# Kernel tuning notes

Measured on AMD Instinct MI355X. Metric: run time of the kernel, lower is better.

Reference implementation:

```python
import jax, jax.numpy as jnp
import numpy as np

# Module hyperparameters (from init_kwargs)
IOU_T = 0.5
PROB_T = 0.75
COV = 10.0
TOPK = 500       # self.topk
PRE_K = 2048     # fixed-shape cap on post-threshold candidates entering NMS
B, C, H, W = 4, 4, 160, 160


def setup_inputs() -> dict:
    key = jax.random.key(0)
    k1, k2 = jax.random.split(key)
    mask = jax.random.normal(k1, (B, C, H, W), dtype=jnp.float32)
    # scale bias so boxes have ~10px extent (realistic detections)
    bias = jax.random.normal(k2, (B, 4, H, W), dtype=jnp.float32) * 8.0
    return {"mask": mask, "bias": bias}


def _pos_grid(h, w):
    # equivalent of np.dstack(np.mgrid[0:h, 0:w]) -> [h, w, 2] with (y, x)
    yy, xx = jnp.meshgrid(jnp.arange(h), jnp.arange(w), indexing="ij")
    return jnp.stack([yy, xx], axis=-1).astype(jnp.float32)


def _pairwise_iou(b):
    # b: [K, 4] as (y1, x1, y2, x2); torchvision-style IoU (areas unclamped, inter clamped)
    area = (b[:, 2] - b[:, 0]) * (b[:, 3] - b[:, 1])
    lt = jnp.maximum(b[:, None, :2], b[None, :, :2])
    rb = jnp.minimum(b[:, None, 2:], b[None, :, 2:])
    wh = jnp.clip(rb - lt, 0.0)
    inter = wh[..., 0] * wh[..., 1]
    return inter / (area[:, None] + area[None, :] - inter)


def _nms_keep(iou, valid, thresh):
    # boxes are pre-sorted by descending score; greedy suppression
    K = iou.shape[0]
    idx = jnp.arange(K)
    def body(i, keep):
        sup = (iou[i] > thresh) & (idx > i) & keep[i]
        return keep & ~sup
    return jax.lax.fori_loop(0, K, body, valid)


def _per_image(mask_i, bias_i, pos):
    # mask_i: [C, h, w], bias_i: [4, h, w], pos: [h, w, 2]
    p = jax.nn.softmax(mask_i, axis=0)
    prob = jax.lax.stop_gradient(p.max(axis=0))          # prob.detach()
    cls = p.argmax(axis=0)
    frontal = (cls != 0) & (prob > PROB_T)               # [h, w]
    # boxes = pos tiled to (y,x,y,x) + bias.permute(0,2,3,1)
    boxes = jnp.concatenate([pos, pos], axis=-1) + jnp.transpose(bias_i, (1, 2, 0))
    boxes = boxes.reshape(-1, 4)                          # [h*w, 4]
    score = jnp.where(frontal.reshape(-1), prob.reshape(-1), -1.0)
    # fixed-size candidate set, sorted by descending score (invalid -> -1)
    top_s, idx = jax.lax.top_k(score, PRE_K)
    cand = boxes[idx]
    valid = top_s > 0.0                                   # valid scores > PROB_T > 0
    keep = _nms_keep(_pairwise_iou(cand), valid, IOU_T)
    kept_s = jnp.where(keep, top_s, -1.0)
    fin_s, fi = jax.lax.top_k(kept_s, TOPK)               # min(topk, n) via padding
    fboxes = cand[fi]                                     # [TOPK, 4]
    fvalid = fin_s > 0.0
    fprob = jnp.where(fvalid, fin_s, 0.0)
    mu = (fboxes[:, :2] + fboxes[:, 2:]) * 0.5            # [TOPK, 2]
    sigma = fboxes[:, 2:] - fboxes[:, :2]
    sigma = jnp.where(fvalid[:, None], sigma, 1.0)        # safe divisor for padding
    # gaussian2d: z = (pos - mu) / (sigma / cov); heat = max_n exp(-|z|^2/2) * prob
    z = (pos[None] - mu[:, None, None, :]) / (sigma[:, None, None, :] / COV)  # [TOPK,h,w,2]
    g = jnp.exp(-0.5 * (z ** 2).sum(axis=-1)) * fprob[:, None, None]
    heat = g.max(axis=0)                                  # [h, w]; all-padded -> 0, matches n==0 case
    return heat, fboxes, fvalid


def reference(mask, bias):
    pos = _pos_grid(mask.shape[2], mask.shape[3])
    heat, fboxes, fvalid = jax.vmap(lambda m, b: _per_image(m, b, pos))(mask, bias)
    # original returns (heatmaps, mask, boxes); boxes padded to [B, TOPK, 4] with validity mask
    return heat, mask, fboxes, fvalid
```

## Files before the change

### kernel.cpp

```cpp
#include <hip/hip_runtime.h>
#include <math.h>

#define BATCH 4
#define NCH 4
#define H 160
#define W 160
#define NPIX (H * W)
#define PRE_K 2048
#define TOPK 500
#define PROB_T 0.75f
#define IOU_T 0.5f
#define COV 10.0f

#define SCORE_OFF 0u
#define FS_OFF    409600u
#define FIDX_OFF  819200u
#define F_OFF     1228800u
#define CIDX_OFF  1228864u
#define CSC_OFF   1261632u
#define CBOX_OFF  1294400u
#define SUP_OFF   1425472u
#define KEEP_OFF  3522624u
#define NV_OFF    3523648u
#define PAR_OFF   3523712u
#define FLAG_OFF  3563712u

#define OUT_HEAT_OFF 0
#define OUT_MASK_OFF 102400
#define OUT_BOX_OFF  512000
#define OUT_VAL_OFF  520000

typedef unsigned long long u64;
typedef unsigned int u32;

__device__ __forceinline__ int block_scan_excl(int v, int tid, int* tmp, int* total) {
    tmp[tid] = v;
    __syncthreads();
    for (int off = 1; off < 256; off <<= 1) {
        int y = (tid >= off) ? tmp[tid - off] : 0;
        __syncthreads();
        tmp[tid] += y;
        __syncthreads();
    }
    int incl = tmp[tid];
    *total = tmp[255];
    __syncthreads();
    return incl - v;
}

__global__ void k_score(const float* __restrict__ mask, float* __restrict__ score) {
    int b = blockIdx.y;
    int pix = blockIdx.x * 256 + threadIdx.x;
    const float* mp = mask + (size_t)b * NCH * NPIX + pix;
    float x0 = mp[0], x1 = mp[NPIX], x2 = mp[2 * NPIX], x3 = mp[3 * NPIX];
    float m = x0; int c = 0;
    if (x1 > m) { m = x1; c = 1; }
    if (x2 > m) { m = x2; c = 2; }
    if (x3 > m) { m = x3; c = 3; }
    float sum = ((expf(x0 - m) + expf(x1 - m)) + expf(x2 - m)) + expf(x3 - m);
    float prob = 1.0f / sum;
    bool frontal = (c != 0) && (prob > PROB_T);
    score[(size_t)b * NPIX + pix] = frontal ? prob : -1.0f;
}

#define PPT (NPIX / 1024)
__global__ void __launch_bounds__(1024)
k_compact(const float* __restrict__ score, float* __restrict__ fs,
          int* __restrict__ fidx, int* __restrict__ Fout,
          int* __restrict__ cand_idx, float* __restrict__ cand_score) {
    int b = blockIdx.x;
    int tid = threadIdx.x;
    const float* sc = score + (size_t)b * NPIX;
    int p0 = tid * PPT;
    float v[PPT];
    int cnt = 0;
    #pragma unroll
    for (int j = 0; j < PPT; ++j) {
        v[j] = sc[p0 + j];
        cnt += (v[j] > 0.0f) ? 1 : 0;
    }
    int lane = tid & 63, wv = tid >> 6;
    int incl = cnt;
    for (int off = 1; off < 64; off <<= 1) {
        int y = __shfl_up(incl, off);
        if (lane >= off) incl += y;
    }
    __shared__ int wtot[16];
    __shared__ int wpre[17];
    if (lane == 63) wtot[wv] = incl;
    __syncthreads();
    if (tid == 0) {
        int acc = 0;
        for (int k = 0; k < 16; ++k) { wpre[k] = acc; acc += wtot[k]; }
        wpre[16] = acc;
    }
    __syncthreads();
    int f_excl = wpre[wv] + (incl - cnt);
    int F = wpre[16];
    if (tid == 0) Fout[b] = F;
    int w = f_excl;
    #pragma unroll
    for (int j = 0; j < PPT; ++j) {
        if (v[j] > 0.0f) {
            fs[(size_t)b * NPIX + w] = v[j];
            fidx[(size_t)b * NPIX + w] = p0 + j;
            ++w;
        }
    }
    if (F < PRE_K) {
        int slot = F + (p0 - f_excl);
        if (slot < PRE_K) {
            #pragma unroll
            for (int j = 0; j < PPT; ++j) {
                if (!(v[j] > 0.0f)) {
                    if (slot < PRE_K) {
                        cand_idx[(size_t)b * PRE_K + slot] = p0 + j;
                        cand_score[(size_t)b * PRE_K + slot] = -1.0f;
                    }
                    ++slot;
                }
            }
        }
    }
}

__global__ void k_rank(const float* __restrict__ fs, const int* __restrict__ fidx,
                       const int* __restrict__ Fout, int* __restrict__ cand_idx,
                       float* __restrict__ cand_score) {
    int b = blockIdx.y;
    int F = Fout[b];
    if (blockIdx.x * 256 >= F) return;
    int i = blockIdx.x * 256 + threadIdx.x;
    bool act = i < F;
    float si = 0.0f; int xi = 0;
    if (act) { si = fs[(size_t)b * NPIX + i]; xi = fidx[(size_t)b * NPIX + i]; }
    int rank = 0;
    __shared__ float ls[256];
    __shared__ int li[256];
    for (int base = 0; base < F; base += 256) {
        int j = base + threadIdx.x;
        if (j < F) { ls[threadIdx.x] = fs[(size_t)b * NPIX + j]; li[threadIdx.x] = fidx[(size_t)b * NPIX + j]; }
        __syncthreads();
        int lim = min(256, F - base);
        if (act) {
            for (int k = 0; k < lim; ++k) {
                float sj = ls[k]; int xj = li[k];
                rank += (sj > si || (sj == si && xj < xi)) ? 1 : 0;
            }
        }
        __syncthreads();
    }
    if (act && rank < PRE_K) {
        cand_idx[(size_t)b * PRE_K + rank] = xi;
        cand_score[(size_t)b * PRE_K + rank] = si;
    }
}

__global__ void k_boxes(const float* __restrict__ bias, const int* __restrict__ cand_idx,
                        float* __restrict__ cand_box) {
    int t = blockIdx.x * 256 + threadIdx.x;
    int b = t >> 11;
    int s = t & (PRE_K - 1);
    int pix = cand_idx[(size_t)b * PRE_K + s];
    float y = (float)(pix / W), x = (float)(pix % W);
    const float* bb = bias + (size_t)b * 4 * NPIX;
    float4 box;
    box.x = y + bb[0 * NPIX + pix];
    box.y = x + bb[1 * NPIX + pix];
    box.z = y + bb[2 * NPIX + pix];
    box.w = x + bb[3 * NPIX + pix];
    ((float4*)cand_box)[(size_t)b * PRE_K + s] = box;
}

__global__ void __launch_bounds__(512)
k_iou(const float* __restrict__ cand_box, u32* __restrict__ sup,
      unsigned char* __restrict__ flag) {
    int b = blockIdx.y;
    int r0 = blockIdx.x * 8;
    __shared__ float ly1[PRE_K], lx1[PRE_K], ly2[PRE_K], lx2[PRE_K], lar[PRE_K];
    for (int k = threadIdx.x; k < PRE_K; k += 512) {
        float4 v = ((const float4*)cand_box)[(size_t)b * PRE_K + k];
        ly1[k] = v.x; lx1[k] = v.y; ly2[k] = v.z; lx2[k] = v.w;
        lar[k] = (v.z - v.x) * (v.w - v.y);
    }
    __syncthreads();
    int lr = threadIdx.x >> 6;
    int w = threadIdx.x & 63;
    int i = r0 + lr;
    float ay1 = ly1[i], ax1 = lx1[i], ay2 = ly2[i], ax2 = lx2[i], aa = lar[i];
    u32 bits = 0;
    int jbase = w * 32;
    #pragma unroll 4
    for (int jj = 0; jj < 32; ++jj) {
        int jo = (jj + w) & 31;
        int j = jbase + jo;
        if (j > i) {
            float lty = fmaxf(ay1, ly1[j]);
            float ltx = fmaxf(ax1, lx1[j]);
            float rby = fminf(ay2, ly2[j]);
            float rbx = fminf(ax2, lx2[j]);
            float wy = fmaxf(rby - lty, 0.0f);
            float wx = fmaxf(rbx - ltx, 0.0f);
            float inter = wy * wx;
            float iou = inter / ((aa + lar[j]) - inter);
            if (iou > IOU_T) bits |= (1u << jo);
        }
    }
    sup[((size_t)b * PRE_K + i) * 64 + w] = bits;
    bool any = __any(bits != 0u);
    if (w == 0) flag[(size_t)b * PRE_K + i] = any ? 1 : 0;
}

__global__ void __launch_bounds__(64)
k_nms(const u32* __restrict__ sup, const unsigned char* __restrict__ flag,
      const int* __restrict__ Fout, u32* __restrict__ keep) {
    int b = blockIdx.x;
    int lane = threadIdx.x;
    int F = Fout[b];
    int V = F < PRE_K ? F : PRE_K;
    __shared__ int rid_s[PRE_K];

    const u32* f32 = (const u32*)(flag + (size_t)b * PRE_K);
    u32 fw[8];
    #pragma unroll
    for (int k = 0; k < 8; ++k) fw[k] = f32[lane * 8 + k];
    int r0 = lane * 32;
    int cnt = 0;
    #pragma unroll
    for (int k = 0; k < 8; ++k) {
        #pragma unroll
        for (int j = 0; j < 4; ++j) {
            int r = r0 + k * 4 + j;
            if (((fw[k] >> (8 * j)) & 0xFFu) != 0u && r < V) ++cnt;
        }
    }
    int incl = cnt;
    for (int off = 1; off < 64; off <<= 1) {
        int y = __shfl_up(incl, off);
        if (lane >= off) incl += y;
    }
    int M = __shfl(incl, 63);
    int pos = incl - cnt;
    #pragma unroll
    for (int k = 0; k < 8; ++k) {
        #pragma unroll
        for (int j = 0; j < 4; ++j) {
            int r = r0 + k * 4 + j;
            if (((fw[k] >> (8 * j)) & 0xFFu) != 0u && r < V) rid_s[pos++] = r;
        }
    }
    __syncthreads();

    int rem = V - lane * 32;
    u32 kw = (rem >= 32) ? 0xFFFFFFFFu : (rem <= 0 ? 0u : ((1u << rem) - 1u));

    const u32* supb = sup + (size_t)b * PRE_K * 64 + lane;
    int C = (M + 7) >> 3;
    int C4 = (C + 3) & ~3;
    int l7 = lane & 7;

    u32 rbuf[4][8];
    int ridv[4];

    #define LOAD_RID(slot, c) ridv[slot] = rid_s[min((c) * 8 + l7, PRE_K - 1)]
    #define ISSUE(slot) do { \
        _Pragma("unroll") \
        for (int k_ = 0; k_ < 8; ++k_) { \
            int i_ = __builtin_amdgcn_readlane(ridv[slot], k_) & (PRE_K - 1); \
            rbuf[slot][k_] = supb[(size_t)i_ * 64]; \
        } \
    } while (0)
    #define PROC(slot, c) do { \
        _Pragma("unroll") \
        for (int k_ = 0; k_ < 8; ++k_) { \
            int m_ = (c) * 8 + k_; \
            if (m_ < M) { \
                int i_ = __builtin_amdgcn_readlane(ridv[slot], k_) & (PRE_K - 1); \
                u32 kb_ = (u32)__builtin_amdgcn_readlane((int)kw, i_ >> 5); \
                if ((kb_ >> (i_ & 31)) & 1u) kw &= ~rbuf[slot][k_]; \
            } \
        } \
    } while (0)

    LOAD_RID(0, 0); LOAD_RID(1, 1); LOAD_RID(2, 2); LOAD_RID(3, 3);
    ISSUE(0); ISSUE(1); ISSUE(2);

    for (int c = 0; c < C4; c += 4) {
        PROC(0, c);     ISSUE(3);            LOAD_RID(0, c + 4);
        PROC(1, c + 1); ISSUE(0);            LOAD_RID(1, c + 5);
        PROC(2, c + 2); ISSUE(1);            LOAD_RID(2, c + 6);
        PROC(3, c + 3); ISSUE(2);            LOAD_RID(3, c + 7);
    }
    #undef LOAD_RID
    #undef ISSUE
    #undef PROC

    keep[(size_t)b * 64 + lane] = kw;
}

__global__ void k_finalize(const u32* __restrict__ keep, const float* __restrict__ cand_score,
                           const float* __restrict__ cand_box, float* __restrict__ out_boxes,
                           float* __restrict__ out_valid, float* __restrict__ params,
                           int* __restrict__ NV) {
    int b = blockIdx.x;
    int tid = threadIdx.x;
    __shared__ u32 kws[64];
    __shared__ int tmp[256];
    if (tid < 64) kws[tid] = keep[(size_t)b * 64 + tid];
    __syncthreads();
    int s0 = tid * 8;
    int bits8 = (int)((kws[s0 >> 5] >> (s0 & 31)) & 0xFFu);
    int cnt = __popc(bits8);
    int tot;
    int kpre = block_scan_excl(cnt, tid, tmp, &tot);
    int NK = tot;
    for (int k = 0; k < 8; ++k) {
        int s = s0 + k;
        int kept = (bits8 >> k) & 1;
        int pos = kept ? kpre : (NK + s - kpre);
        if (pos < TOPK) {
            float4 bx = ((const float4*)cand_box)[(size_t)b * PRE_K + s];
            ((float4*)out_boxes)[(size_t)b * TOPK + pos] = bx;
            out_valid[(size_t)b * TOPK + pos] = kept ? 1.0f : 0.0f;
            if (kept) {
                float scv = cand_score[(size_t)b * PRE_K + s];
                float* pp = params + ((size_t)b * TOPK + pos) * 5;
                pp[0] = (bx.x + bx.z) * 0.5f;
                pp[1] = (bx.y + bx.w) * 0.5f;
                pp[2] = (bx.z - bx.x) / COV;
                pp[3] = (bx.w - bx.y) / COV;
                pp[4] = scv;
            }
        }
        kpre += kept;
    }
    if (tid == 0) NV[b] = NK < TOPK ? NK : TOPK;
}

#define TILE 16
#define TPL (W / TILE)
__global__ void k_heat(const float* __restrict__ params, const int* __restrict__ NV,
                       float* __restrict__ heat) {
    int b = blockIdx.y;
    int ty0 = (blockIdx.x / TPL) * TILE;
    int tx0 = (blockIdx.x % TPL) * TILE;
    int tid = threadIdx.x;
    int nv = NV[b];
    __shared__ float lp[TOPK * 5];
    __shared__ int cntS;
    if (tid == 0) cntS = 0;
    __syncthreads();
    for (int t = tid; t < nv; t += 256) {
        const float* pp = params + ((size_t)b * TOPK + t) * 5;
        float muy = pp[0], mux = pp[1], dy = pp[2], dx = pp[3], p = pp[4];
        float cy = fmaxf(fmaxf((float)ty0 - muy, muy - (float)(ty0 + TILE - 1)), 0.0f);
        float cx = fmaxf(fmaxf((float)tx0 - mux, mux - (float)(tx0 + TILE - 1)), 0.0f);
        float zy = cy / fabsf(dy);
        float zx = cx / fabsf(dx);
        float z2 = zy * zy + zx * zx;
        if (!(z2 > 40.0f)) {
            int idx = atomicAdd(&cntS, 1);
            float* q = lp + idx * 5;
            q[0] = muy; q[1] = mux; q[2] = dy; q[3] = dx; q[4] = p;
        }
    }
    __syncthreads();
    int n = cntS;
    float py = (float)(ty0 + (tid >> 4));
    float px = (float)(tx0 + (tid & 15));
    float m = 0.0f;
    for (int t = 0; t < n; ++t) {
        float muy = lp[t * 5 + 0], mux = lp[t * 5 + 1];
        float dy = lp[t * 5 + 2], dx = lp[t * 5 + 3], p = lp[t * 5 + 4];
        float zy = (py - muy) / dy;
        float zx = (px - mux) / dx;
        float g = expf(-0.5f * (zy * zy + zx * zx)) * p;
        m = fmaxf(m, g);
    }
    heat[(size_t)b * NPIX + (ty0 + (tid >> 4)) * W + tx0 + (tid & 15)] = m;
}

extern "C" void kernel_launch(void* const* d_in, const int* in_sizes, int n_in,
                              void* d_out, int out_size, void* d_ws, size_t ws_size,
                              hipStream_t stream) {
    const float* mask = (const float*)d_in[0];
    const float* bias = (const float*)d_in[1];
    float* out = (float*)d_out;
    char* ws = (char*)d_ws;

    float* score      = (float*)(ws + SCORE_OFF);
    float* fs         = (float*)(ws + FS_OFF);
    int*   fidx       = (int*)(ws + FIDX_OFF);
    int*   Fout       = (int*)(ws + F_OFF);
    int*   cand_idx   = (int*)(ws + CIDX_OFF);
    float* cand_score = (float*)(ws + CSC_OFF);
    float* cand_box   = (float*)(ws + CBOX_OFF);
    u32*   sup        = (u32*)(ws + SUP_OFF);
    u32*   keep       = (u32*)(ws + KEEP_OFF);
    int*   NV         = (int*)(ws + NV_OFF);
    float* params     = (float*)(ws + PAR_OFF);
    unsigned char* flag = (unsigned char*)(ws + FLAG_OFF);

    hipMemcpyAsync(out + OUT_MASK_OFF, mask, (size_t)BATCH * NCH * NPIX * sizeof(float),
                   hipMemcpyDeviceToDevice, stream);

    dim3 g100(NPIX / 256, BATCH);
    k_score<<<g100, 256, 0, stream>>>(mask, score);
    k_compact<<<BATCH, 1024, 0, stream>>>(score, fs, fidx, Fout, cand_idx, cand_score);
    k_rank<<<g100, 256, 0, stream>>>(fs, fidx, Fout, cand_idx, cand_score);
    k_boxes<<<dim3(BATCH * PRE_K / 256), 256, 0, stream>>>(bias, cand_idx, cand_box);
    k_iou<<<dim3(PRE_K / 8, BATCH), 512, 0, stream>>>(cand_box, sup, flag);
    k_nms<<<BATCH, 64, 0, stream>>>(sup, flag, Fout, keep);
    k_finalize<<<BATCH, 256, 0, stream>>>(keep, cand_score, cand_box,
                                          out + OUT_BOX_OFF, out + OUT_VAL_OFF, params, NV);
    k_heat<<<dim3(TPL * (H / TILE), BATCH), 256, 0, stream>>>(params, NV, out + OUT_HEAT_OFF);
}
```

Baseline: 137.7 us.

## Fuse pipeline stages and drop memcpy, skip IoU rows beyond valid count

Folds the mask copy into the score kernel, merges compaction, ranking and box gathering into one per-image kernel that ranks candidates from LDS, and merges NMS with finalize. IoU blocks whose rows all fall past the valid candidate count now exit early. This cuts launches, intermediate global traffic and wasted IoU work. The cost is that ranking now runs in only one 1024-thread block per image, which serialises O(F^2) comparisons when there are many candidates.

```diff
diff --git a/kernel.cpp b/kernel.cpp
--- a/kernel.cpp
+++ b/kernel.cpp
@@ -11,6 +11,7 @@
 #define PROB_T 0.75f
 #define IOU_T 0.5f
 #define COV 10.0f
+#define CAP 4096
 
 #define SCORE_OFF 0u
 #define FS_OFF    409600u
@@ -20,7 +21,6 @@
 #define CSC_OFF   1261632u
 #define CBOX_OFF  1294400u
 #define SUP_OFF   1425472u
-#define KEEP_OFF  3522624u
 #define NV_OFF    3523648u
 #define PAR_OFF   3523712u
 #define FLAG_OFF  3563712u
@@ -48,11 +48,14 @@
     return incl - v;
 }
 
-__global__ void k_score(const float* __restrict__ mask, float* __restrict__ score) {
+__global__ void k_score(const float* __restrict__ mask, float* __restrict__ score,
+                        float* __restrict__ out_mask) {
     int b = blockIdx.y;
     int pix = blockIdx.x * 256 + threadIdx.x;
     const float* mp = mask + (size_t)b * NCH * NPIX + pix;
+    float* op = out_mask + (size_t)b * NCH * NPIX + pix;
     float x0 = mp[0], x1 = mp[NPIX], x2 = mp[2 * NPIX], x3 = mp[3 * NPIX];
+    op[0] = x0; op[NPIX] = x1; op[2 * NPIX] = x2; op[3 * NPIX] = x3;
     float m = x0; int c = 0;
     if (x1 > m) { m = x1; c = 1; }
     if (x2 > m) { m = x2; c = 2; }
@@ -65,12 +68,14 @@
 
 #define PPT (NPIX / 1024)
 __global__ void __launch_bounds__(1024)
-k_compact(const float* __restrict__ score, float* __restrict__ fs,
-          int* __restrict__ fidx, int* __restrict__ Fout,
-          int* __restrict__ cand_idx, float* __restrict__ cand_score) {
+k_select(const float* __restrict__ score, const float* __restrict__ bias,
+         float* __restrict__ fs, int* __restrict__ fidx, int* __restrict__ Fout,
+         int* __restrict__ cand_idx, float* __restrict__ cand_score,
+         float* __restrict__ cand_box) {
     int b = blockIdx.x;
     int tid = threadIdx.x;
     const float* sc = score + (size_t)b * NPIX;
+    const float* bb = bias + (size_t)b * 4 * NPIX;
     int p0 = tid * PPT;
     float v[PPT];
     int cnt = 0;
@@ -87,6 +92,8 @@
     }
     __shared__ int wtot[16];
     __shared__ int wpre[17];
+    __shared__ float fs_l[CAP];
+    __shared__ int fi_l[CAP];
     if (lane == 63) wtot[wv] = incl;
     __syncthreads();
     if (tid == 0) {
@@ -104,79 +111,71 @@
         if (v[j] > 0.0f) {
             fs[(size_t)b * NPIX + w] = v[j];
             fidx[(size_t)b * NPIX + w] = p0 + j;
+            if (w < CAP) { fs_l[w] = v[j]; fi_l[w] = p0 + j; }
             ++w;
         }
     }
     if (F < PRE_K) {
         int slot = F + (p0 - f_excl);
-        if (slot < PRE_K) {
-            #pragma unroll
-            for (int j = 0; j < PPT; ++j) {
-                if (!(v[j] > 0.0f)) {
-                    if (slot < PRE_K) {
-                        cand_idx[(size_t)b * PRE_K + slot] = p0 + j;
-                        cand_score[(size_t)b * PRE_K + slot] = -1.0f;
-                    }
-                    ++slot;
+        #pragma unroll
+        for (int j = 0; j < PPT; ++j) {
+            if (!(v[j] > 0.0f)) {
+                if (slot < PRE_K) {
+                    int pix = p0 + j;
+                    cand_idx[(size_t)b * PRE_K + slot] = pix;
+                    cand_score[(size_t)b * PRE_K + slot] = -1.0f;
+                    float y = (float)(pix / W), x = (float)(pix % W);
+                    float4 box;
+                    box.x = y + bb[0 * NPIX + pix];
+                    box.y = x + bb[1 * NPIX + pix];
+                    box.z = y + bb[2 * NPIX + pix];
+                    box.w = x + bb[3 * NPIX + pix];
+                    ((float4*)cand_box)[(size_t)b * PRE_K + slot] = box;
                 }
-            }
-        }
-    }
-}
-
-__global__ void k_rank(const float* __restrict__ fs, const int* __restrict__ fidx,
-                       const int* __restrict__ Fout, int* __restrict__ cand_idx,
-                       float* __restrict__ cand_score) {
+                ++slot;
+            }
+        }
+    }
+    __syncthreads();
+    bool lds = (F <= CAP);
+    for (int i = tid; i < F; i += 1024) {
+        float si; int xi;
+        if (lds) { si = fs_l[i]; xi = fi_l[i]; }
+        else     { si = fs[(size_t)b * NPIX + i]; xi = fidx[(size_t)b * NPIX + i]; }
+        int rank = 0;
+        if (lds) {
+            for (int k = 0; k < F; ++k) {
+                float sj = fs_l[k]; int xj = fi_l[k];
+                rank += (sj > si || (sj == si && xj < xi)) ? 1 : 0;
+            }
+        } else {
+            for (int k = 0; k < F; ++k) {
+                float sj = fs[(size_t)b * NPIX + k]; int xj = fidx[(size_t)b * NPIX + k];
+                rank += (sj > si || (sj == si && xj < xi)) ? 1 : 0;
+            }
+        }
+        if (rank < PRE_K) {
+            cand_idx[(size_t)b * PRE_K + rank] = xi;
+            cand_score[(size_t)b * PRE_K + rank] = si;
+            float y = (float)(xi / W), x = (float)(xi % W);
+            float4 box;
+            box.x = y + bb[0 * NPIX + xi];
+            box.y = x + bb[1 * NPIX + xi];
+            box.z = y + bb[2 * NPIX + xi];
+            box.w = x + bb[3 * NPIX + xi];
+            ((float4*)cand_box)[(size_t)b * PRE_K + rank] = box;
+        }
+    }
+}
+
+__global__ void __launch_bounds__(512)
+k_iou(const float* __restrict__ cand_box, const int* __restrict__ Fout,
+      u32* __restrict__ sup, unsigned char* __restrict__ flag) {
     int b = blockIdx.y;
     int F = Fout[b];
-    if (blockIdx.x * 256 >= F) return;
-    int i = blockIdx.x * 256 + threadIdx.x;
-    bool act = i < F;
-    float si = 0.0f; int xi = 0;
-    if (act) { si = fs[(size_t)b * NPIX + i]; xi = fidx[(size_t)b * NPIX + i]; }
-    int rank = 0;
-    __shared__ float ls[256];
-    __shared__ int li[256];
-    for (int base = 0; base < F; base += 256) {
-        int j = base + threadIdx.x;
-        if (j < F) { ls[threadIdx.x] = fs[(size_t)b * NPIX + j]; li[threadIdx.x] = fidx[(size_t)b * NPIX + j]; }
-        __syncthreads();
-        int lim = min(256, F - base);
-        if (act) {
-            for (int k = 0; k < lim; ++k) {
-                float sj = ls[k]; int xj = li[k];
-                rank += (sj > si || (sj == si && xj < xi)) ? 1 : 0;
-            }
-        }
-        __syncthreads();
-    }
-    if (act && rank < PRE_K) {
-        cand_idx[(size_t)b * PRE_K + rank] = xi;
-        cand_score[(size_t)b * PRE_K + rank] = si;
-    }
-}
-
-__global__ void k_boxes(const float* __restrict__ bias, const int* __restrict__ cand_idx,
-                        float* __restrict__ cand_box) {
-    int t = blockIdx.x * 256 + threadIdx.x;
-    int b = t >> 11;
-    int s = t & (PRE_K - 1);
-    int pix = cand_idx[(size_t)b * PRE_K + s];
-    float y = (float)(pix / W), x = (float)(pix % W);
-    const float* bb = bias + (size_t)b * 4 * NPIX;
-    float4 box;
-    box.x = y + bb[0 * NPIX + pix];
-    box.y = x + bb[1 * NPIX + pix];
-    box.z = y + bb[2 * NPIX + pix];
-    box.w = x + bb[3 * NPIX + pix];
-    ((float4*)cand_box)[(size_t)b * PRE_K + s] = box;
-}
-
-__global__ void __launch_bounds__(512)
-k_iou(const float* __restrict__ cand_box, u32* __restrict__ sup,
-      unsigned char* __restrict__ flag) {
-    int b = blockIdx.y;
+    int V = F < PRE_K ? F : PRE_K;
     int r0 = blockIdx.x * 8;
+    if (r0 >= V) return;
     __shared__ float ly1[PRE_K], lx1[PRE_K], ly2[PRE_K], lx2[PRE_K], lar[PRE_K];
     for (int k = threadIdx.x; k < PRE_K; k += 512) {
         float4 v = ((const float4*)cand_box)[(size_t)b * PRE_K + k];
@@ -211,103 +210,100 @@
     if (w == 0) flag[(size_t)b * PRE_K + i] = any ? 1 : 0;
 }
 
-__global__ void __launch_bounds__(64)
-k_nms(const u32* __restrict__ sup, const unsigned char* __restrict__ flag,
-      const int* __restrict__ Fout, u32* __restrict__ keep) {
+__global__ void __launch_bounds__(256)
+k_nmsfin(const u32* __restrict__ sup, const unsigned char* __restrict__ flag,
+         const int* __restrict__ Fout, const float* __restrict__ cand_score,
+         const float* __restrict__ cand_box, float* __restrict__ out_boxes,
+         float* __restrict__ out_valid, float* __restrict__ params,
+         int* __restrict__ NV) {
     int b = blockIdx.x;
-    int lane = threadIdx.x;
+    int tid = threadIdx.x;
     int F = Fout[b];
     int V = F < PRE_K ? F : PRE_K;
     __shared__ int rid_s[PRE_K];
-
-    const u32* f32 = (const u32*)(flag + (size_t)b * PRE_K);
-    u32 fw[8];
-    #pragma unroll
-    for (int k = 0; k < 8; ++k) fw[k] = f32[lane * 8 + k];
-    int r0 = lane * 32;
-    int cnt = 0;
-    #pragma unroll
-    for (int k = 0; k < 8; ++k) {
-        #pragma unroll
-        for (int j = 0; j < 4; ++j) {
-            int r = r0 + k * 4 + j;
-            if (((fw[k] >> (8 * j)) & 0xFFu) != 0u && r < V) ++cnt;
-        }
-    }
-    int incl = cnt;
-    for (int off = 1; off < 64; off <<= 1) {
-        int y = __shfl_up(incl, off);
-        if (lane >= off) incl += y;
-    }
-    int M = __shfl(incl, 63);
-    int pos = incl - cnt;
-    #pragma unroll
-    for (int k = 0; k < 8; ++k) {
-        #pragma unroll
-        for (int j = 0; j < 4; ++j) {
-            int r = r0 + k * 4 + j;
-            if (((fw[k] >> (8 * j)) & 0xFFu) != 0u && r < V) rid_s[pos++] = r;
-        }
-    }
-    __syncthreads();
-
-    int rem = V - lane * 32;
-    u32 kw = (rem >= 32) ? 0xFFFFFFFFu : (rem <= 0 ? 0u : ((1u << rem) - 1u));
-
-    const u32* supb = sup + (size_t)b * PRE_K * 64 + lane;
-    int C = (M + 7) >> 3;
-    int C4 = (C + 3) & ~3;
-    int l7 = lane & 7;
-
-    u32 rbuf[4][8];
-    int ridv[4];
-
-    #define LOAD_RID(slot, c) ridv[slot] = rid_s[min((c) * 8 + l7, PRE_K - 1)]
-    #define ISSUE(slot) do { \
-        _Pragma("unroll") \
-        for (int k_ = 0; k_ < 8; ++k_) { \
-            int i_ = __builtin_amdgcn_readlane(ridv[slot], k_) & (PRE_K - 1); \
-            rbuf[slot][k_] = supb[(size_t)i_ * 64]; \
-        } \
-    } while (0)
-    #define PROC(slot, c) do { \
-        _Pragma("unroll") \
-        for (int k_ = 0; k_ < 8; ++k_) { \
-            int m_ = (c) * 8 + k_; \
-            if (m_ < M) { \
-                int i_ = __builtin_amdgcn_readlane(ridv[slot], k_) & (PRE_K - 1); \
-                u32 kb_ = (u32)__builtin_amdgcn_readlane((int)kw, i_ >> 5); \
-                if ((kb_ >> (i_ & 31)) & 1u) kw &= ~rbuf[slot][k_]; \
-            } \
-        } \
-    } while (0)
-
-    LOAD_RID(0, 0); LOAD_RID(1, 1); LOAD_RID(2, 2); LOAD_RID(3, 3);
-    ISSUE(0); ISSUE(1); ISSUE(2);
-
-    for (int c = 0; c < C4; c += 4) {
-        PROC(0, c);     ISSUE(3);            LOAD_RID(0, c + 4);
-        PROC(1, c + 1); ISSUE(0);            LOAD_RID(1, c + 5);
-        PROC(2, c + 2); ISSUE(1);            LOAD_RID(2, c + 6);
-        PROC(3, c + 3); ISSUE(2);            LOAD_RID(3, c + 7);
-    }
-    #undef LOAD_RID
-    #undef ISSUE
-    #undef PROC
-
-    keep[(size_t)b * 64 + lane] = kw;
-}
-
-__global__ void k_finalize(const u32* __restrict__ keep, const float* __restrict__ cand_score,
-                           const float* __restrict__ cand_box, float* __restrict__ out_boxes,
-                           float* __restrict__ out_valid, float* __restrict__ params,
-                           int* __restrict__ NV) {
-    int b = blockIdx.x;
-    int tid = threadIdx.x;
+    __shared__ int M_s;
     __shared__ u32 kws[64];
     __shared__ int tmp[256];
-    if (tid < 64) kws[tid] = keep[(size_t)b * 64 + tid];
-    __syncthreads();
+
+    if (tid < 64) {
+        int lane = tid;
+        const u32* f32 = (const u32*)(flag + (size_t)b * PRE_K);
+        u32 fw[8];
+        #pragma unroll
+        for (int k = 0; k < 8; ++k) fw[k] = f32[lane * 8 + k];
+        int r0 = lane * 32;
+        int cnt = 0;
+        #pragma unroll
+        for (int k = 0; k < 8; ++k)
+            #pragma unroll
+            for (int j = 0; j < 4; ++j) {
+                int r = r0 + k * 4 + j;
+                if (((fw[k] >> (8 * j)) & 0xFFu) != 0u && r < V) ++cnt;
+            }
+        int incl = cnt;
+        for (int off = 1; off < 64; off <<= 1) {
+            int y = __shfl_up(incl, off);
+            if (lane >= off) incl += y;
+        }
+        if (lane == 63) M_s = incl;
+        int pos = incl - cnt;
+        #pragma unroll
+        for (int k = 0; k < 8; ++k)
+            #pragma unroll
+            for (int j = 0; j < 4; ++j) {
+                int r = r0 + k * 4 + j;
+                if (((fw[k] >> (8 * j)) & 0xFFu) != 0u && r < V) rid_s[pos++] = r;
+            }
+    }
+    __syncthreads();
+
+    if (tid < 64) {
+        int lane = tid;
+        int M = M_s;
+        int rem = V - lane * 32;
+        u32 kw = (rem >= 32) ? 0xFFFFFFFFu : (rem <= 0 ? 0u : ((1u << rem) - 1u));
+        const u32* supb = sup + (size_t)b * PRE_K * 64 + lane;
+        int C = (M + 7) >> 3;
+        int C4 = (C + 3) & ~3;
+        int l7 = lane & 7;
+        u32 rbuf[4][8];
+        int ridv[4];
+
+        #define LOAD_RID(slot, c) ridv[slot] = rid_s[min((c) * 8 + l7, PRE_K - 1)]
+        #define ISSUE(slot) do { \
+            _Pragma("unroll") \
+            for (int k_ = 0; k_ < 8; ++k_) { \
+                int i_ = __builtin_amdgcn_readlane(ridv[slot], k_) & (PRE_K - 1); \
+                rbuf[slot][k_] = supb[(size_t)i_ * 64]; \
+            } \
+        } while (0)
+        #define PROC(slot, c) do { \
+            _Pragma("unroll") \
+            for (int k_ = 0; k_ < 8; ++k_) { \
+                int m_ = (c) * 8 + k_; \
+                if (m_ < M) { \
+                    int i_ = __builtin_amdgcn_readlane(ridv[slot], k_) & (PRE_K - 1); \
+                    u32 kb_ = (u32)__builtin_amdgcn_readlane((int)kw, i_ >> 5); \
+                    if ((kb_ >> (i_ & 31)) & 1u) kw &= ~rbuf[slot][k_]; \
+                } \
+            } \
+        } while (0)
+
+        LOAD_RID(0, 0); LOAD_RID(1, 1); LOAD_RID(2, 2); LOAD_RID(3, 3);
+        ISSUE(0); ISSUE(1); ISSUE(2);
+        for (int c = 0; c < C4; c += 4) {
+            PROC(0, c);     ISSUE(3);            LOAD_RID(0, c + 4);
+            PROC(1, c + 1); ISSUE(0);            LOAD_RID(1, c + 5);
+            PROC(2, c + 2); ISSUE(1);            LOAD_RID(2, c + 6);
+            PROC(3, c + 3); ISSUE(2);            LOAD_RID(3, c + 7);
+        }
+        #undef LOAD_RID
+        #undef ISSUE
+        #undef PROC
+        kws[lane] = kw;
+    }
+    __syncthreads();
+
     int s0 = tid * 8;
     int bits8 = (int)((kws[s0 >> 5] >> (s0 & 31)) & 0xFFu);
     int cnt = __popc(bits8);
@@ -396,22 +392,16 @@
     float* cand_score = (float*)(ws + CSC_OFF);
     float* cand_box   = (float*)(ws + CBOX_OFF);
     u32*   sup        = (u32*)(ws + SUP_OFF);
-    u32*   keep       = (u32*)(ws + KEEP_OFF);
     int*   NV         = (int*)(ws + NV_OFF);
     float* params     = (float*)(ws + PAR_OFF);
     unsigned char* flag = (unsigned char*)(ws + FLAG_OFF);
 
-    hipMemcpyAsync(out + OUT_MASK_OFF, mask, (size_t)BATCH * NCH * NPIX * sizeof(float),
-                   hipMemcpyDeviceToDevice, stream);
-
     dim3 g100(NPIX / 256, BATCH);
-    k_score<<<g100, 256, 0, stream>>>(mask, score);
-    k_compact<<<BATCH, 1024, 0, stream>>>(score, fs, fidx, Fout, cand_idx, cand_score);
-    k_rank<<<g100, 256, 0, stream>>>(fs, fidx, Fout, cand_idx, cand_score);
-    k_boxes<<<dim3(BATCH * PRE_K / 256), 256, 0, stream>>>(bias, cand_idx, cand_box);
-    k_iou<<<dim3(PRE_K / 8, BATCH), 512, 0, stream>>>(cand_box, sup, flag);
-    k_nms<<<BATCH, 64, 0, stream>>>(sup, flag, Fout, keep);
-    k_finalize<<<BATCH, 256, 0, stream>>>(keep, cand_score, cand_box,
-                                          out + OUT_BOX_OFF, out + OUT_VAL_OFF, params, NV);
+    k_score<<<g100, 256, 0, stream>>>(mask, score, out + OUT_MASK_OFF);
+    k_select<<<BATCH, 1024, 0, stream>>>(score, bias, fs, fidx, Fout,
+                                         cand_idx, cand_score, cand_box);
+    k_iou<<<dim3(PRE_K / 8, BATCH), 512, 0, stream>>>(cand_box, Fout, sup, flag);
+    k_nmsfin<<<BATCH, 256, 0, stream>>>(sup, flag, Fout, cand_score, cand_box,
+                                        out + OUT_BOX_OFF, out + OUT_VAL_OFF, params, NV);
     k_heat<<<dim3(TPL * (H / TILE), BATCH), 256, 0, stream>>>(params, NV, out + OUT_HEAT_OFF);
 }
```

After: 340.6 us. 147% more time.
